# Performance work log

Hardware: AMD Instinct MI355X
Metric: run time of the kernel (lower is better)

Reference implementation:

```python
import jax, jax.numpy as jnp
import numpy as np

B, L, D_ENC = 32, 512, 512
STEPS = 32
E_DIM = 128      # embedding_dim
A_DIM = 256      # attention_dim
H = 512          # hidden_size
VOCAB = 32000


def _linear(x, W, b):
    return x @ W.T + b


def setup_inputs() -> dict:
    key = jax.random.key(0)
    ks = jax.random.split(key, 12)
    s = lambda fan_in: 1.0 / np.sqrt(fan_in)
    return {
        "encoder_outputs": jax.random.normal(ks[0], (B, L, D_ENC), dtype=jnp.float32),
        "target_seq": jax.random.randint(ks[1], (B, STEPS), 0, VOCAB, dtype=jnp.int64),
        "pos_embedding": jax.random.normal(ks[2], (STEPS, E_DIM), dtype=jnp.float32),
        "dec_proj_W": jax.random.uniform(ks[3], (A_DIM, E_DIM), minval=-s(E_DIM), maxval=s(E_DIM)),
        "dec_proj_b": jnp.zeros((A_DIM,), jnp.float32),
        "enc_proj_W": jax.random.uniform(ks[4], (A_DIM, D_ENC), minval=-s(D_ENC), maxval=s(D_ENC)),
        "enc_proj_b": jnp.zeros((A_DIM,), jnp.float32),
        "attn_score_W": jax.random.uniform(ks[5], (1, A_DIM), minval=-s(A_DIM), maxval=s(A_DIM)),
        "attn_score_b": jnp.zeros((1,), jnp.float32),
        "hidden_proj_W": jax.random.uniform(ks[6], (H, E_DIM), minval=-s(E_DIM), maxval=s(E_DIM)),
        "hidden_proj_b": jnp.zeros((H,), jnp.float32),
        "fc_out_W": jax.random.uniform(ks[7], (VOCAB, H + D_ENC), minval=-s(H + D_ENC), maxval=s(H + D_ENC)),
        "fc_out_b": jnp.zeros((VOCAB,), jnp.float32),
    }


def reference(encoder_outputs, target_seq, pos_embedding,
              dec_proj_W, dec_proj_b, enc_proj_W, enc_proj_b,
              attn_score_W, attn_score_b, hidden_proj_W, hidden_proj_b,
              fc_out_W, fc_out_b):
    batch = encoder_outputs.shape[0]
    steps = target_seq.shape[1]
    # [B, L, A]
    enc_proj = _linear(encoder_outputs, enc_proj_W, enc_proj_b)
    # [B, S, E]  (dropout=0 in eval)
    pos_emb = jnp.broadcast_to(pos_embedding[:steps][None], (batch, steps, pos_embedding.shape[1]))
    # [B, S, A]
    dec_query = _linear(pos_emb, dec_proj_W, dec_proj_b)
    # additive attention: [B, S, L, A]
    combined = jnp.tanh(enc_proj[:, None, :, :] + dec_query[:, :, None, :])
    # score reduction to scalar: [B, S, L]
    attn_scores = jnp.einsum('bsla,a->bsl', combined, attn_score_W[0]) + attn_score_b[0]
    attn_weights = jax.nn.softmax(attn_scores, axis=2)
    # context: [B, S, D_enc]
    context = jnp.einsum('bsl,bld->bsd', attn_weights, encoder_outputs)
    hidden = _linear(pos_emb, hidden_proj_W, hidden_proj_b)  # [B, S, H]
    logits = _linear(jnp.concatenate([hidden, context], axis=-1), fc_out_W, fc_out_b)
    return logits
```

## Files before the change

### kernel.cpp

```cpp
#include <hip/hip_runtime.h>
#include <hip/hip_bf16.h>
#include <stdint.h>

typedef __attribute__((ext_vector_type(4))) float f32x4;
typedef __attribute__((ext_vector_type(8))) short short8;

#define B_   32
#define L_   512
#define DE_  512
#define S_   32
#define ED_  128
#define AD_  256
#define HD_  512
#define VOC_ 32000
#define M_   1024

__device__ __forceinline__ unsigned short f2bf(float f){
  union { float f; unsigned int u; } v; v.f = f;
  unsigned int u = v.u;
  unsigned int r = (u + 0x7FFFu + ((u >> 16) & 1u)) >> 16;
  return (unsigned short)r;
}

__device__ __forceinline__ float bf2f(unsigned short u){
  union { unsigned int u; float f; } v; v.u = ((unsigned int)u) << 16;
  return v.f;
}

__device__ __forceinline__ float tanh_fast(float x){
  float t = __expf(2.0f * x);
  return (t - 1.0f) * __builtin_amdgcn_rcpf(t + 1.0f);
}

__device__ __forceinline__ void gl_lds16(const void* g, void* l){
  __builtin_amdgcn_global_load_lds(
      (const __attribute__((address_space(1))) unsigned int*)g,
      (__attribute__((address_space(3))) unsigned int*)l, 16, 0, 0);
}

extern "C" __global__ void __launch_bounds__(256)
k_cvt(const float* __restrict__ src, unsigned short* __restrict__ dst, int n4){
  int stride = gridDim.x * 256;
  for (int i = blockIdx.x * 256 + threadIdx.x; i < n4; i += stride){
    f32x4 v = ((const f32x4*)src)[i];
    ushort4 o;
    o.x = f2bf(v[0]); o.y = f2bf(v[1]); o.z = f2bf(v[2]); o.w = f2bf(v[3]);
    ((ushort4*)dst)[i] = o;
  }
}

extern "C" __global__ void __launch_bounds__(256)
k_cvtW(const float* __restrict__ fcW, unsigned short* __restrict__ Wc, int n4){
  int stride = gridDim.x * 256;
  for (int i = blockIdx.x * 256 + threadIdx.x; i < n4; i += stride){
    int row = i >> 7;
    int c4  = i & 127;
    f32x4 v = *(const f32x4*)&fcW[(size_t)row * 1024 + 512 + c4 * 4];
    ushort4 o;
    o.x = f2bf(v[0]); o.y = f2bf(v[1]); o.z = f2bf(v[2]); o.w = f2bf(v[3]);
    *(ushort4*)&Wc[(size_t)row * 512 + c4 * 4] = o;
  }
}

extern "C" __global__ void __launch_bounds__(256)
k_small(const float* __restrict__ pos, const float* __restrict__ dW, const float* __restrict__ db,
        const float* __restrict__ hW, const float* __restrict__ hb,
        float* __restrict__ dq, unsigned short* __restrict__ hbf){
  int t = blockIdx.x * 256 + threadIdx.x;
  if (t < S_ * AD_){
    int s = t >> 8, a = t & 255;
    const float* p = pos + s * ED_;
    const float* wrow = dW + a * ED_;
    float acc = db[a];
    #pragma unroll 4
    for (int e = 0; e < ED_; ++e) acc += p[e] * wrow[e];
    dq[t] = acc;
  } else if (t < S_ * AD_ + S_ * HD_){
    int u = t - S_ * AD_;
    int s = u >> 9, h = u & 511;
    const float* p = pos + s * ED_;
    const float* wrow = hW + h * ED_;
    float acc = hb[h];
    #pragma unroll 4
    for (int e = 0; e < ED_; ++e) acc += p[e] * wrow[e];
    hbf[u] = f2bf(acc);
  }
}

extern "C" __global__ void __launch_bounds__(256)
k_gemm_encp(const unsigned short* __restrict__ A, const unsigned short* __restrict__ Bt,
            const float* __restrict__ bias, unsigned short* __restrict__ C){
  __shared__ unsigned short As[128 * 32];
  __shared__ unsigned short Bs[128 * 32];
  int bm = blockIdx.x >> 1, bn = blockIdx.x & 1;
  int tid = threadIdx.x, wid = tid >> 6, lane = tid & 63;
  int fr = lane & 15, fq = lane >> 4;
  int wm = wid >> 1, wn = wid & 1;
  f32x4 acc[4][4];
  #pragma unroll
  for (int i = 0; i < 4; ++i)
    #pragma unroll
    for (int j = 0; j < 4; ++j) acc[i][j] = (f32x4)0.0f;

  for (int k0 = 0; k0 < 512; k0 += 32){
    __syncthreads();
    #pragma unroll
    for (int i = 0; i < 2; ++i){
      int seg = wid * 2 + i;
      int row = seg * 16 + (lane >> 2);
      int col = (lane & 3) * 8;
      gl_lds16(A  + (size_t)(bm * 128 + row) * 512 + k0 + col, &As[seg * 512]);
      gl_lds16(Bt + (size_t)(bn * 128 + row) * 512 + k0 + col, &Bs[seg * 512]);
    }
    __syncthreads();
    short8 a[4], b[4];
    #pragma unroll
    for (int mf = 0; mf < 4; ++mf) a[mf] = *(const short8*)&As[(wm * 64 + mf * 16 + fr) * 32 + fq * 8];
    #pragma unroll
    for (int nf = 0; nf < 4; ++nf) b[nf] = *(const short8*)&Bs[(wn * 64 + nf * 16 + fr) * 32 + fq * 8];
    #pragma unroll
    for (int mf = 0; mf < 4; ++mf)
      #pragma unroll
      for (int nf = 0; nf < 4; ++nf)
        acc[mf][nf] = __builtin_amdgcn_mfma_f32_16x16x32_bf16(a[mf], b[nf], acc[mf][nf], 0, 0, 0);
  }
  #pragma unroll
  for (int mf = 0; mf < 4; ++mf){
    int row = bm * 128 + wm * 64 + mf * 16 + fq * 4;
    #pragma unroll
    for (int nf = 0; nf < 4; ++nf){
      int col = bn * 128 + wn * 64 + nf * 16 + fr;
      float bv = bias[col];
      #pragma unroll
      for (int j = 0; j < 4; ++j)
        C[(size_t)(row + j) * 256 + col] = f2bf(acc[mf][nf][j] + bv);
    }
  }
}

extern "C" __global__ void __launch_bounds__(256)
k_attn(const unsigned short* __restrict__ encp, const float* __restrict__ dq,
       const float* __restrict__ vW, float* __restrict__ wgt){
  int idx = blockIdx.x;
  int wg = (idx & 7) * 128 + (idx >> 3);
  int b = wg >> 5, s = wg & 31;
  int tid = threadIdx.x, wid = tid >> 6, lane = tid & 63;
  int half = lane >> 5, a0 = (lane & 31) * 8;
  __shared__ float sc[512];
  __shared__ float redm[4], reds[4];
  f32x4 dqa = *(const f32x4*)&dq[s * AD_ + a0];
  f32x4 dqb = *(const f32x4*)&dq[s * AD_ + a0 + 4];
  f32x4 va  = *(const f32x4*)&vW[a0];
  f32x4 vb  = *(const f32x4*)&vW[a0 + 4];
  for (int it = 0; it < 64; ++it){
    int l = wid * 128 + it * 2 + half;
    short8 e8 = *(const short8*)&encp[((size_t)(b * 512 + l)) * 256 + a0];
    float p = 0.0f;
    #pragma unroll
    for (int j = 0; j < 4; ++j) p += tanh_fast(bf2f((unsigned short)e8[j]) + dqa[j]) * va[j];
    #pragma unroll
    for (int j = 0; j < 4; ++j) p += tanh_fast(bf2f((unsigned short)e8[4 + j]) + dqb[j]) * vb[j];
    #pragma unroll
    for (int off = 16; off >= 1; off >>= 1) p += __shfl_xor(p, off);
    if ((lane & 31) == 0) sc[l] = p;
  }
  __syncthreads();
  float s0 = sc[tid], s1 = sc[tid + 256];
  float m = fmaxf(s0, s1);
  #pragma unroll
  for (int off = 32; off >= 1; off >>= 1) m = fmaxf(m, __shfl_xor(m, off));
  if (lane == 0) redm[wid] = m;
  __syncthreads();
  m = fmaxf(fmaxf(redm[0], redm[1]), fmaxf(redm[2], redm[3]));
  float e0 = __expf(s0 - m), e1 = __expf(s1 - m);
  float sum = e0 + e1;
  #pragma unroll
  for (int off = 32; off >= 1; off >>= 1) sum += __shfl_xor(sum, off);
  if (lane == 0) reds[wid] = sum;
  __syncthreads();
  float tot = reds[0] + reds[1] + reds[2] + reds[3];
  float inv = __builtin_amdgcn_rcpf(tot);
  size_t base = (size_t)(b * 32 + s) * 512;
  wgt[base + tid] = e0 * inv;
  wgt[base + tid + 256] = e1 * inv;
}

extern "C" __global__ void __launch_bounds__(256)
k_ctx(const float* __restrict__ enc, const float* __restrict__ wgt, unsigned short* __restrict__ ctx){
  int b = blockIdx.x >> 4, dt = blockIdx.x & 15;
  int tid = threadIdx.x;
  __shared__ float wl[32 * 512];
  #pragma unroll 8
  for (int i = 0; i < 64; ++i)
    wl[i * 256 + tid] = wgt[(size_t)b * 16384 + i * 256 + tid];
  __syncthreads();
  int d = dt * 32 + (tid & 31);
  int grp = tid >> 5;
  float acc0 = 0, acc1 = 0, acc2 = 0, acc3 = 0;
  const float* ebase = enc + (size_t)b * 262144 + d;
  const float* w0 = &wl[(grp * 4 + 0) * 512];
  const float* w1 = &wl[(grp * 4 + 1) * 512];
  const float* w2 = &wl[(grp * 4 + 2) * 512];
  const float* w3 = &wl[(grp * 4 + 3) * 512];
  #pragma unroll 8
  for (int l = 0; l < 512; ++l){
    float e = ebase[(size_t)l * 512];
    acc0 += w0[l] * e; acc1 += w1[l] * e; acc2 += w2[l] * e; acc3 += w3[l] * e;
  }
  size_t obase = (size_t)(b * 32 + grp * 4) * 512 + d;
  ctx[obase]        = f2bf(acc0);
  ctx[obase + 512]  = f2bf(acc1);
  ctx[obase + 1024] = f2bf(acc2);
  ctx[obase + 1536] = f2bf(acc3);
}

extern "C" __global__ void __launch_bounds__(256)
k_logh(const unsigned short* __restrict__ hbf, const float* __restrict__ fcW,
       const float* __restrict__ fcb, float* __restrict__ logh){
  int bn = blockIdx.x;
  int tid = threadIdx.x, wid = tid >> 6, lane = tid & 63;
  int fr = lane & 15, fq = lane >> 4;
  int col = bn * 64 + wid * 16 + fr;
  const float* brow = fcW + (size_t)col * 1024;
  f32x4 acc0 = (f32x4)0.0f, acc1 = (f32x4)0.0f;
  #pragma unroll 4
  for (int k0 = 0; k0 < 512; k0 += 32){
    int ko = k0 + fq * 8;
    f32x4 b0 = *(const f32x4*)(brow + ko);
    f32x4 b1 = *(const f32x4*)(brow + ko + 4);
    short8 bfr;
    bfr[0] = (short)f2bf(b0[0]); bfr[1] = (short)f2bf(b0[1]);
    bfr[2] = (short)f2bf(b0[2]); bfr[3] = (short)f2bf(b0[3]);
    bfr[4] = (short)f2bf(b1[0]); bfr[5] = (short)f2bf(b1[1]);
    bfr[6] = (short)f2bf(b1[2]); bfr[7] = (short)f2bf(b1[3]);
    short8 a0 = *(const short8*)&hbf[(size_t)fr * 512 + ko];
    short8 a1 = *(const short8*)&hbf[(size_t)(16 + fr) * 512 + ko];
    acc0 = __builtin_amdgcn_mfma_f32_16x16x32_bf16(a0, bfr, acc0, 0, 0, 0);
    acc1 = __builtin_amdgcn_mfma_f32_16x16x32_bf16(a1, bfr, acc1, 0, 0, 0);
  }
  float bv = fcb[col];
  #pragma unroll
  for (int j = 0; j < 4; ++j){
    logh[(size_t)(fq * 4 + j) * VOC_ + col]      = acc0[j] + bv;
    logh[(size_t)(16 + fq * 4 + j) * VOC_ + col] = acc1[j] + bv;
  }
}

extern "C" __global__ void __launch_bounds__(512, 2)
k_gemm_main(const unsigned short* __restrict__ Abf, const unsigned short* __restrict__ Wc,
            const float* __restrict__ logh, float* __restrict__ out){
  __shared__ unsigned short As[2][256 * 32];
  __shared__ unsigned short Bs[2][256 * 32];
  int orig = blockIdx.x;
  int xcd = orig & 7, j = orig >> 3;
  int wgid = (xcd < 4 ? xcd * 63 : 252 + (xcd - 4) * 62) + j;
  int bm = wgid & 3, bn = wgid >> 2;
  int tid = threadIdx.x, wid = tid >> 6, lane = tid & 63;
  int fr = lane & 15, fq = lane >> 4;
  int wm = wid >> 2, wn = wid & 3;
  int abase = bm * 256, bbase = bn * 256;
  int srow = (lane >> 2), scol = (lane & 3) * 8;

  f32x4 acc[8][4];
  #pragma unroll
  for (int i = 0; i < 8; ++i)
    #pragma unroll
    for (int jj = 0; jj < 4; ++jj) acc[i][jj] = (f32x4)0.0f;

  {
    int c0 = wid * 2;
    gl_lds16(Abf + (size_t)(abase + c0 * 16 + srow) * 512 + scol,        &As[0][c0 * 512]);
    gl_lds16(Abf + (size_t)(abase + c0 * 16 + 16 + srow) * 512 + scol,   &As[0][c0 * 512 + 512]);
    gl_lds16(Wc  + (size_t)(bbase + c0 * 16 + srow) * 512 + scol,        &Bs[0][c0 * 512]);
    gl_lds16(Wc  + (size_t)(bbase + c0 * 16 + 16 + srow) * 512 + scol,   &Bs[0][c0 * 512 + 512]);
  }
  __syncthreads();

  int cur = 0;
  for (int t = 0; t < 16; ++t){
    if (t < 15){
      int k0n = (t + 1) * 32;
      int c0 = wid * 2;
      gl_lds16(Abf + (size_t)(abase + c0 * 16 + srow) * 512 + k0n + scol,      &As[cur ^ 1][c0 * 512]);
      gl_lds16(Abf + (size_t)(abase + c0 * 16 + 16 + srow) * 512 + k0n + scol, &As[cur ^ 1][c0 * 512 + 512]);
      gl_lds16(Wc  + (size_t)(bbase + c0 * 16 + srow) * 512 + k0n + scol,      &Bs[cur ^ 1][c0 * 512]);
      gl_lds16(Wc  + (size_t)(bbase + c0 * 16 + 16 + srow) * 512 + k0n + scol, &Bs[cur ^ 1][c0 * 512 + 512]);
    }
    short8 a[8], b[4];
    #pragma unroll
    for (int mf = 0; mf < 8; ++mf)
      a[mf] = *(const short8*)&As[cur][(wm * 128 + mf * 16 + fr) * 32 + fq * 8];
    #pragma unroll
    for (int nf = 0; nf < 4; ++nf)
      b[nf] = *(const short8*)&Bs[cur][(wn * 64 + nf * 16 + fr) * 32 + fq * 8];
    #pragma unroll
    for (int mf = 0; mf < 8; ++mf)
      #pragma unroll
      for (int nf = 0; nf < 4; ++nf)
        acc[mf][nf] = __builtin_amdgcn_mfma_f32_16x16x32_bf16(a[mf], b[nf], acc[mf][nf], 0, 0, 0);
    __syncthreads();
    cur ^= 1;
  }

  #pragma unroll
  for (int mf = 0; mf < 8; ++mf){
    int rowb = bm * 256 + wm * 128 + mf * 16 + fq * 4;
    #pragma unroll
    for (int nf = 0; nf < 4; ++nf){
      int col = bn * 256 + wn * 64 + nf * 16 + fr;
      #pragma unroll
      for (int jj = 0; jj < 4; ++jj){
        int r = rowb + jj;
        out[(size_t)r * VOC_ + col] = acc[mf][nf][jj] + logh[(size_t)(r & 31) * VOC_ + col];
      }
    }
  }
}

extern "C" void kernel_launch(void* const* d_in, const int* in_sizes, int n_in,
                              void* d_out, int out_size, void* d_ws, size_t ws_size,
                              hipStream_t stream){
  const float* enc = (const float*)d_in[0];
  const float* pos = (const float*)d_in[2];
  const float* dW  = (const float*)d_in[3];
  const float* db  = (const float*)d_in[4];
  const float* eW  = (const float*)d_in[5];
  const float* eb  = (const float*)d_in[6];
  const float* vW  = (const float*)d_in[7];
  const float* hW  = (const float*)d_in[9];
  const float* hb  = (const float*)d_in[10];
  const float* fcW = (const float*)d_in[11];
  const float* fcb = (const float*)d_in[12];
  float* out = (float*)d_out;

  char* w = (char*)d_ws;
  unsigned short* Wc_bf   = (unsigned short*)(w);
  unsigned short* enc_bf  = (unsigned short*)(w + 32768000);
  unsigned short* encp_bf = (unsigned short*)(w + 49545216);
  unsigned short* ctx     = (unsigned short*)(w + 57933824);
  float*          logh    = (float*)(w + 58982400);
  float*          dq      = (float*)(w + 63078400);
  unsigned short* hbf     = (unsigned short*)(w + 63111168);
  unsigned short* encW_bf = (unsigned short*)(w + 63143936);
  float*          wgt     = (float*)(w + 63406080);

  k_cvt<<<dim3(2048), dim3(256), 0, stream>>>(enc, enc_bf, 8388608 / 4);
  k_cvt<<<dim3(128), dim3(256), 0, stream>>>(eW, encW_bf, 131072 / 4);
  k_cvtW<<<dim3(2048), dim3(256), 0, stream>>>(fcW, Wc_bf, 32000 * 512 / 4);
  k_small<<<dim3(96), dim3(256), 0, stream>>>(pos, dW, db, hW, hb, dq, hbf);
  k_gemm_encp<<<dim3(256), dim3(256), 0, stream>>>(enc_bf, encW_bf, eb, encp_bf);
  k_attn<<<dim3(1024), dim3(256), 0, stream>>>(encp_bf, dq, vW, wgt);
  k_ctx<<<dim3(512), dim3(256), 0, stream>>>(enc, wgt, ctx);
  k_logh<<<dim3(500), dim3(256), 0, stream>>>(hbf, fcW, fcb, logh);
  k_gemm_main<<<dim3(500), dim3(512), 0, stream>>>(ctx, Wc_bf, logh, out);
}
```

Baseline: 231.1 us.

## Fuse fc weight conversion into logh kernel, swizzle LDS, deepen gemm prefetch

The separate fc_out weight conversion kernel is folded into the logh kernel, which converts its 64-row slice of the context half of fcW to bf16 while it computes the hidden-part logits. This removes one launch and lets both jobs share the fcW reads. The context kernel now reads the bf16 copy of the encoder outputs, halving its load bytes at some precision cost. The main GEMM gains an XOR-swizzled LDS layout to reduce bank conflicts, issues loads two tiles ahead with explicit vmcnt waits and raw barriers, and drops its occupancy hint from 2 to 1 block per SIMD.

Result: slower. 238.4 us (+3.2%).

```diff
diff --git a/kernel.cpp b/kernel.cpp
--- a/kernel.cpp
+++ b/kernel.cpp
@@ -46,19 +46,6 @@
     ushort4 o;
     o.x = f2bf(v[0]); o.y = f2bf(v[1]); o.z = f2bf(v[2]); o.w = f2bf(v[3]);
     ((ushort4*)dst)[i] = o;
-  }
-}
-
-extern "C" __global__ void __launch_bounds__(256)
-k_cvtW(const float* __restrict__ fcW, unsigned short* __restrict__ Wc, int n4){
-  int stride = gridDim.x * 256;
-  for (int i = blockIdx.x * 256 + threadIdx.x; i < n4; i += stride){
-    int row = i >> 7;
-    int c4  = i & 127;
-    f32x4 v = *(const f32x4*)&fcW[(size_t)row * 1024 + 512 + c4 * 4];
-    ushort4 o;
-    o.x = f2bf(v[0]); o.y = f2bf(v[1]); o.z = f2bf(v[2]); o.w = f2bf(v[3]);
-    *(ushort4*)&Wc[(size_t)row * 512 + c4 * 4] = o;
   }
 }
 
@@ -186,7 +173,8 @@
 }
 
 extern "C" __global__ void __launch_bounds__(256)
-k_ctx(const float* __restrict__ enc, const float* __restrict__ wgt, unsigned short* __restrict__ ctx){
+k_ctx(const unsigned short* __restrict__ encb, const float* __restrict__ wgt,
+      unsigned short* __restrict__ ctx){
   int b = blockIdx.x >> 4, dt = blockIdx.x & 15;
   int tid = threadIdx.x;
   __shared__ float wl[32 * 512];
@@ -197,14 +185,14 @@
   int d = dt * 32 + (tid & 31);
   int grp = tid >> 5;
   float acc0 = 0, acc1 = 0, acc2 = 0, acc3 = 0;
-  const float* ebase = enc + (size_t)b * 262144 + d;
+  const unsigned short* ebase = encb + (size_t)b * 262144 + d;
   const float* w0 = &wl[(grp * 4 + 0) * 512];
   const float* w1 = &wl[(grp * 4 + 1) * 512];
   const float* w2 = &wl[(grp * 4 + 2) * 512];
   const float* w3 = &wl[(grp * 4 + 3) * 512];
   #pragma unroll 8
   for (int l = 0; l < 512; ++l){
-    float e = ebase[(size_t)l * 512];
+    float e = bf2f(ebase[(size_t)l * 512]);
     acc0 += w0[l] * e; acc1 += w1[l] * e; acc2 += w2[l] * e; acc3 += w3[l] * e;
   }
   size_t obase = (size_t)(b * 32 + grp * 4) * 512 + d;
@@ -215,11 +203,21 @@
 }
 
 extern "C" __global__ void __launch_bounds__(256)
-k_logh(const unsigned short* __restrict__ hbf, const float* __restrict__ fcW,
-       const float* __restrict__ fcb, float* __restrict__ logh){
+k_wprep(const float* __restrict__ fcW, const unsigned short* __restrict__ hbf,
+        const float* __restrict__ fcb, unsigned short* __restrict__ Wc,
+        float* __restrict__ logh){
   int bn = blockIdx.x;
   int tid = threadIdx.x, wid = tid >> 6, lane = tid & 63;
   int fr = lane & 15, fq = lane >> 4;
+  #pragma unroll 8
+  for (int i = 0; i < 32; ++i){
+    int idx = i * 256 + tid;
+    int row = idx >> 7, c4 = idx & 127;
+    f32x4 v = *(const f32x4*)&fcW[(size_t)(bn * 64 + row) * 1024 + 512 + c4 * 4];
+    ushort4 o;
+    o.x = f2bf(v[0]); o.y = f2bf(v[1]); o.z = f2bf(v[2]); o.w = f2bf(v[3]);
+    *(ushort4*)&Wc[(size_t)(bn * 64 + row) * 512 + c4 * 4] = o;
+  }
   int col = bn * 64 + wid * 16 + fr;
   const float* brow = fcW + (size_t)col * 1024;
   f32x4 acc0 = (f32x4)0.0f, acc1 = (f32x4)0.0f;
@@ -246,7 +244,7 @@
   }
 }
 
-extern "C" __global__ void __launch_bounds__(512, 2)
+extern "C" __global__ void __launch_bounds__(512, 1)
 k_gemm_main(const unsigned short* __restrict__ Abf, const unsigned short* __restrict__ Wc,
             const float* __restrict__ logh, float* __restrict__ out){
   __shared__ unsigned short As[2][256 * 32];
@@ -259,7 +257,14 @@
   int fr = lane & 15, fq = lane >> 4;
   int wm = wid >> 2, wn = wid & 3;
   int abase = bm * 256, bbase = bn * 256;
-  int srow = (lane >> 2), scol = (lane & 3) * 8;
+  int srow = lane >> 2;
+  int scol = ((lane & 3) ^ ((lane >> 3) & 3)) * 8;
+  int c0 = wid * 2;
+  const unsigned short* aS0 = Abf + (size_t)(abase + c0 * 16 + srow) * 512 + scol;
+  const unsigned short* aS1 = aS0 + (size_t)16 * 512;
+  const unsigned short* bS0 = Wc  + (size_t)(bbase + c0 * 16 + srow) * 512 + scol;
+  const unsigned short* bS1 = bS0 + (size_t)16 * 512;
+  int swzfq = (fq ^ ((fr >> 1) & 3)) * 8;
 
   f32x4 acc[8][4];
   #pragma unroll
@@ -267,40 +272,48 @@
     #pragma unroll
     for (int jj = 0; jj < 4; ++jj) acc[i][jj] = (f32x4)0.0f;
 
-  {
-    int c0 = wid * 2;
-    gl_lds16(Abf + (size_t)(abase + c0 * 16 + srow) * 512 + scol,        &As[0][c0 * 512]);
-    gl_lds16(Abf + (size_t)(abase + c0 * 16 + 16 + srow) * 512 + scol,   &As[0][c0 * 512 + 512]);
-    gl_lds16(Wc  + (size_t)(bbase + c0 * 16 + srow) * 512 + scol,        &Bs[0][c0 * 512]);
-    gl_lds16(Wc  + (size_t)(bbase + c0 * 16 + 16 + srow) * 512 + scol,   &Bs[0][c0 * 512 + 512]);
-  }
-  __syncthreads();
+#define STAGE_MAIN(buf, kk) do { \
+    gl_lds16(aS0 + (kk), &As[buf][c0 * 512]); \
+    gl_lds16(aS1 + (kk), &As[buf][c0 * 512 + 512]); \
+    gl_lds16(bS0 + (kk), &Bs[buf][c0 * 512]); \
+    gl_lds16(bS1 + (kk), &Bs[buf][c0 * 512 + 512]); \
+  } while (0)
+
+  STAGE_MAIN(0, 0);
+  STAGE_MAIN(1, 32);
+  asm volatile("s_waitcnt vmcnt(4)" ::: "memory");
+  __builtin_amdgcn_s_barrier();
+  __builtin_amdgcn_sched_barrier(0);
 
   int cur = 0;
   for (int t = 0; t < 16; ++t){
-    if (t < 15){
-      int k0n = (t + 1) * 32;
-      int c0 = wid * 2;
-      gl_lds16(Abf + (size_t)(abase + c0 * 16 + srow) * 512 + k0n + scol,      &As[cur ^ 1][c0 * 512]);
-      gl_lds16(Abf + (size_t)(abase + c0 * 16 + 16 + srow) * 512 + k0n + scol, &As[cur ^ 1][c0 * 512 + 512]);
-      gl_lds16(Wc  + (size_t)(bbase + c0 * 16 + srow) * 512 + k0n + scol,      &Bs[cur ^ 1][c0 * 512]);
-      gl_lds16(Wc  + (size_t)(bbase + c0 * 16 + 16 + srow) * 512 + k0n + scol, &Bs[cur ^ 1][c0 * 512 + 512]);
-    }
     short8 a[8], b[4];
     #pragma unroll
     for (int mf = 0; mf < 8; ++mf)
-      a[mf] = *(const short8*)&As[cur][(wm * 128 + mf * 16 + fr) * 32 + fq * 8];
+      a[mf] = *(const short8*)&As[cur][(wm * 128 + mf * 16 + fr) * 32 + swzfq];
     #pragma unroll
     for (int nf = 0; nf < 4; ++nf)
-      b[nf] = *(const short8*)&Bs[cur][(wn * 64 + nf * 16 + fr) * 32 + fq * 8];
+      b[nf] = *(const short8*)&Bs[cur][(wn * 64 + nf * 16 + fr) * 32 + swzfq];
     #pragma unroll
     for (int mf = 0; mf < 8; ++mf)
       #pragma unroll
       for (int nf = 0; nf < 4; ++nf)
         acc[mf][nf] = __builtin_amdgcn_mfma_f32_16x16x32_bf16(a[mf], b[nf], acc[mf][nf], 0, 0, 0);
-    __syncthreads();
+    __builtin_amdgcn_s_barrier();
+    __builtin_amdgcn_sched_barrier(0);
+    if (t < 14){
+      STAGE_MAIN(cur, (size_t)(t + 2) * 32);
+      asm volatile("s_waitcnt vmcnt(4)" ::: "memory");
+    } else if (t == 14){
+      asm volatile("s_waitcnt vmcnt(0)" ::: "memory");
+    }
+    if (t < 15){
+      __builtin_amdgcn_s_barrier();
+      __builtin_amdgcn_sched_barrier(0);
+    }
     cur ^= 1;
   }
+#undef STAGE_MAIN
 
   #pragma unroll
   for (int mf = 0; mf < 8; ++mf){
@@ -346,11 +359,10 @@
 
   k_cvt<<<dim3(2048), dim3(256), 0, stream>>>(enc, enc_bf, 8388608 / 4);
   k_cvt<<<dim3(128), dim3(256), 0, stream>>>(eW, encW_bf, 131072 / 4);
-  k_cvtW<<<dim3(2048), dim3(256), 0, stream>>>(fcW, Wc_bf, 32000 * 512 / 4);
   k_small<<<dim3(96), dim3(256), 0, stream>>>(pos, dW, db, hW, hb, dq, hbf);
   k_gemm_encp<<<dim3(256), dim3(256), 0, stream>>>(enc_bf, encW_bf, eb, encp_bf);
   k_attn<<<dim3(1024), dim3(256), 0, stream>>>(encp_bf, dq, vW, wgt);
-  k_ctx<<<dim3(512), dim3(256), 0, stream>>>(enc, wgt, ctx);
-  k_logh<<<dim3(500), dim3(256), 0, stream>>>(hbf, fcW, fcb, logh);
+  k_ctx<<<dim3(512), dim3(256), 0, stream>>>(enc_bf, wgt, ctx);
+  k_wprep<<<dim3(500), dim3(256), 0, stream>>>(fcW, hbf, fcb, Wc_bf, logh);
   k_gemm_main<<<dim3(500), dim3(512), 0, stream>>>(ctx, Wc_bf, logh, out);
 }
```
